# Kernel optimization log

Hardware: AMD Instinct MI355X
Metric: run time of the kernel (lower is better)

Reference implementation:

```python
import jax, jax.numpy as jnp
import numpy as np

NUM_ROUNDS = 3


def squash(x, axis=-1):
    # s_norm / (1 + s_norm) * x / sqrt(s_norm), matching the torch code exactly
    s_norm = jnp.sum(x * x, axis=axis, keepdims=True)
    return (s_norm / (1.0 + s_norm)) * x / jnp.sqrt(s_norm)


def setup_inputs() -> dict:
    key = jax.random.key(0)
    k1, k2 = jax.random.split(key)
    x = jax.random.normal(k1, (512, 1152, 8), dtype=jnp.float32)   # [B, R, Cin]
    W = jax.random.normal(k2, (10, 1152, 8, 16), dtype=jnp.float32)  # [N, R, Cin, Cout]
    return {"x": x, "W": W}


def reference(x, W):
    # priors = x[None,:,:,None,:] @ W[:,None,:,:,:]  -> [N, B, R, 1, Cout]
    priors = jnp.einsum('bri,nrio->nbro', x, W)[:, :, :, None, :]
    logits = jnp.zeros_like(priors)  # [N, B, R, 1, Cout]
    outps = None
    for i in range(NUM_ROUNDS):
        probs = jax.nn.softmax(logits, axis=2)  # softmax over routes R
        outps = squash(jnp.sum(probs * priors, axis=2, keepdims=True))  # [N, B, 1, 1, Cout]
        if i != NUM_ROUNDS - 1:
            # agreement logit update: dot over Cout
            logits = logits + jnp.sum(priors * outps, axis=-1, keepdims=True)
    return outps
```

## Files before the change

kernel.cpp:

```cpp
#include <hip/hip_runtime.h>
#include <math.h>

#define R_ROUTES 1152
#define CIN 8
#define COUT 16
#define BATCH 512
#define NCAPS 10
#define NUM_ROUNDS 3

typedef __fp16 h2 __attribute__((ext_vector_type(2)));
union U32H2 { unsigned int u; h2 h; };

__device__ __forceinline__ unsigned int pkrtz(float lo, float hi) {
    U32H2 v; v.h = __builtin_amdgcn_cvt_pkrtz(lo, hi);
    return v.u;
}
__device__ __forceinline__ h2 as_h2(unsigned int u) { U32H2 v; v.u = u; return v.h; }
__device__ __forceinline__ float f_lo(unsigned int u) { return (float)as_h2(u).x; }
__device__ __forceinline__ float f_hi(unsigned int u) { return (float)as_h2(u).y; }
__device__ __forceinline__ float dot2(unsigned int p, unsigned int s, float c) {
    return __builtin_amdgcn_fdot2(as_h2(p), as_h2(s), c, false);
}

__device__ __forceinline__ int sunit(int r, int h) {
    return (2 * r + h) ^ ((r >> 2) & 7);
}

extern "C" __global__ void __launch_bounds__(512, 4)
capsule_routing_v8(const float* __restrict__ x,
                   const float* __restrict__ W,
                   float* __restrict__ out)
{
    __shared__ unsigned int pbuf[2 * R_ROUTES * 8];
    __shared__ float red[2 * 32 * 20];
    __shared__ float sred[2 * 4];
    __shared__ float sv[2 * 16];

    const int blk = blockIdx.x;
    const int n = blk >> 8;
    const int bp = blk & 255;
    const int t = threadIdx.x;

    const float* __restrict__ x0 = x + (size_t)(2 * bp) * (R_ROUTES * CIN);
    const float* __restrict__ x1 = x0 + R_ROUTES * CIN;
    const float* __restrict__ Wn = W + (size_t)n * (R_ROUTES * CIN * COUT);

    {
        const int q = t >> 2;
        const int oq = t & 3;
        const int subw = (oq & 1) * 2;
        const int hq = oq >> 1;

        #pragma unroll 1
        for (int it = 0; it < 9; ++it) {
            const int r = it * 128 + q;
            const float4* __restrict__ wp = (const float4*)(Wn + (size_t)r * 128) + oq;
            float4 wv[8];
            #pragma unroll
            for (int i = 0; i < 8; ++i) wv[i] = wp[i * 4];
            const float4 xa0 = *(const float4*)(x0 + r * 8);
            const float4 xa1 = *(const float4*)(x0 + r * 8 + 4);
            const float4 xb0 = *(const float4*)(x1 + r * 8);
            const float4 xb1 = *(const float4*)(x1 + r * 8 + 4);

            {
                const float xs[8] = {xa0.x, xa0.y, xa0.z, xa0.w,
                                     xa1.x, xa1.y, xa1.z, xa1.w};
                float a0 = 0.f, a1 = 0.f, a2 = 0.f, a3 = 0.f;
                #pragma unroll
                for (int i = 0; i < 8; ++i) {
                    a0 = fmaf(xs[i], wv[i].x, a0);
                    a1 = fmaf(xs[i], wv[i].y, a1);
                    a2 = fmaf(xs[i], wv[i].z, a2);
                    a3 = fmaf(xs[i], wv[i].w, a3);
                }
                uint2 u; u.x = pkrtz(a0, a1); u.y = pkrtz(a2, a3);
                *(uint2*)(pbuf + sunit(r, hq) * 4 + subw) = u;
            }
            {
                const float xs[8] = {xb0.x, xb0.y, xb0.z, xb0.w,
                                     xb1.x, xb1.y, xb1.z, xb1.w};
                float a0 = 0.f, a1 = 0.f, a2 = 0.f, a3 = 0.f;
                #pragma unroll
                for (int i = 0; i < 8; ++i) {
                    a0 = fmaf(xs[i], wv[i].x, a0);
                    a1 = fmaf(xs[i], wv[i].y, a1);
                    a2 = fmaf(xs[i], wv[i].z, a2);
                    a3 = fmaf(xs[i], wv[i].w, a3);
                }
                uint2 u; u.x = pkrtz(a0, a1); u.y = pkrtz(a2, a3);
                *(uint2*)(pbuf + R_ROUTES * 8 + sunit(r, hq) * 4 + subw) = u;
            }
        }
    }
    __syncthreads();

    const int half = t >> 8;
    const int tt = t & 255;
    unsigned int* __restrict__ pb = pbuf + half * (R_ROUTES * 8);
    float* __restrict__ redh = red + half * (32 * 20);
    float* __restrict__ sredh = sred + half * 4;
    float* __restrict__ svh = sv + half * 16;

    const int nr = (tt < 128) ? 5 : 4;
    float bl[5] = {0.f, 0.f, 0.f, 0.f, 0.f};
    float factor = 0.f;

    for (int pass = 0; pass < NUM_ROUNDS; ++pass) {
        float acc[16];
        #pragma unroll
        for (int o = 0; o < 16; ++o) acc[o] = 0.f;
        float es = 0.f;

        if (pass == 0) {
            #pragma unroll
            for (int k = 0; k < 5; ++k) {
                if (k < nr) {
                    const int r = tt + (k << 8);
                    const uint4 a = *(const uint4*)(pb + sunit(r, 0) * 4);
                    const uint4 c = *(const uint4*)(pb + sunit(r, 1) * 4);
                    acc[0]  += f_lo(a.x); acc[1]  += f_hi(a.x);
                    acc[2]  += f_lo(a.y); acc[3]  += f_hi(a.y);
                    acc[4]  += f_lo(a.z); acc[5]  += f_hi(a.z);
                    acc[6]  += f_lo(a.w); acc[7]  += f_hi(a.w);
                    acc[8]  += f_lo(c.x); acc[9]  += f_hi(c.x);
                    acc[10] += f_lo(c.y); acc[11] += f_hi(c.y);
                    acc[12] += f_lo(c.z); acc[13] += f_hi(c.z);
                    acc[14] += f_lo(c.w); acc[15] += f_hi(c.w);
                }
            }
        } else {
            unsigned int svp[8];
            #pragma unroll
            for (int j = 0; j < 8; ++j)
                svp[j] = pkrtz(svh[2 * j], svh[2 * j + 1]);
            #pragma unroll
            for (int k = 0; k < 5; ++k) {
                if (k < nr) {
                    const int r = tt + (k << 8);
                    const uint4 a = *(const uint4*)(pb + sunit(r, 0) * 4);
                    const uint4 c = *(const uint4*)(pb + sunit(r, 1) * 4);
                    float d = 0.f;
                    d = dot2(a.x, svp[0], d);
                    d = dot2(a.y, svp[1], d);
                    d = dot2(a.z, svp[2], d);
                    d = dot2(a.w, svp[3], d);
                    d = dot2(c.x, svp[4], d);
                    d = dot2(c.y, svp[5], d);
                    d = dot2(c.z, svp[6], d);
                    d = dot2(c.w, svp[7], d);
                    bl[k] = fmaf(factor, d, bl[k]);
                    const float e = __expf(bl[k]);
                    es += e;
                    acc[0]  = fmaf(e, f_lo(a.x), acc[0]);
                    acc[1]  = fmaf(e, f_hi(a.x), acc[1]);
                    acc[2]  = fmaf(e, f_lo(a.y), acc[2]);
                    acc[3]  = fmaf(e, f_hi(a.y), acc[3]);
                    acc[4]  = fmaf(e, f_lo(a.z), acc[4]);
                    acc[5]  = fmaf(e, f_hi(a.z), acc[5]);
                    acc[6]  = fmaf(e, f_lo(a.w), acc[6]);
                    acc[7]  = fmaf(e, f_hi(a.w), acc[7]);
                    acc[8]  = fmaf(e, f_lo(c.x), acc[8]);
                    acc[9]  = fmaf(e, f_hi(c.x), acc[9]);
                    acc[10] = fmaf(e, f_lo(c.y), acc[10]);
                    acc[11] = fmaf(e, f_hi(c.y), acc[11]);
                    acc[12] = fmaf(e, f_lo(c.z), acc[12]);
                    acc[13] = fmaf(e, f_hi(c.z), acc[13]);
                    acc[14] = fmaf(e, f_lo(c.w), acc[14]);
                    acc[15] = fmaf(e, f_hi(c.w), acc[15]);
                }
            }
            #pragma unroll
            for (int off = 32; off > 0; off >>= 1) es += __shfl_xor(es, off, 64);
            if ((t & 63) == 0) sredh[tt >> 6] = es;
        }

        #pragma unroll
        for (int o = 0; o < 16; ++o) {
            acc[o] += __shfl_xor(acc[o], 1, 64);
            acc[o] += __shfl_xor(acc[o], 2, 64);
            acc[o] += __shfl_xor(acc[o], 4, 64);
        }
        if ((tt & 7) == 0) {
            float* dst = redh + (tt >> 3) * 20;
            *(float4*)(dst + 0)  = make_float4(acc[0],  acc[1],  acc[2],  acc[3]);
            *(float4*)(dst + 4)  = make_float4(acc[4],  acc[5],  acc[6],  acc[7]);
            *(float4*)(dst + 8)  = make_float4(acc[8],  acc[9],  acc[10], acc[11]);
            *(float4*)(dst + 12) = make_float4(acc[12], acc[13], acc[14], acc[15]);
        }
        __syncthreads();

        if (tt < 16) {
            float s = 0.f;
            #pragma unroll
            for (int w = 0; w < 32; ++w) s += redh[w * 20 + tt];
            const float Z = (pass == 0)
                ? (float)R_ROUTES
                : (sredh[0] + sredh[1] + sredh[2] + sredh[3]);
            svh[tt] = s / Z;
        }
        __syncthreads();

        float sn = 0.f;
        #pragma unroll
        for (int o = 0; o < 16; ++o) { const float s = svh[o]; sn = fmaf(s, s, sn); }
        factor = sn / ((1.0f + sn) * sqrtf(sn));
    }

    if (tt < 16)
        out[((size_t)n * BATCH + 2 * bp + half) * COUT + tt] = factor * svh[tt];
}

extern "C" void kernel_launch(void* const* d_in, const int* in_sizes, int n_in,
                              void* d_out, int out_size, void* d_ws, size_t ws_size,
                              hipStream_t stream) {
    const float* x = (const float*)d_in[0];
    const float* W = (const float*)d_in[1];
    float* out = (float*)d_out;

    dim3 grid(NCAPS * (BATCH / 2));
    dim3 block(512);
    capsule_routing_v8<<<grid, block, 0, stream>>>(x, W, out);
}
```

Measured before the change: 148.3 us.

## Pre-pack W to fp16 and compute priors with dot2, fold first routing pass

Adds a pack_w kernel that converts W to packed fp16 pairs along Cin, written into the workspace, so the main kernel loads half the W bytes per block and computes priors with fdot2 instead of fp32 FMAs. The uniform first routing pass is folded into the prior-computation loop through per-thread column sums reduced across the wave, which removes one full sweep over the shared prior buffer. Output columns are permuted to match the new per-thread output ordering. The cost is an extra kernel launch and reduced precision on x and W, which are now rounded to fp16 before the products.

```diff
diff --git a/kernel.cpp b/kernel.cpp
--- a/kernel.cpp
+++ b/kernel.cpp
@@ -26,12 +26,28 @@
     return (2 * r + h) ^ ((r >> 2) & 7);
 }
 
+extern "C" __global__ void __launch_bounds__(256)
+pack_w(const float* __restrict__ W, unsigned int* __restrict__ Wp)
+{
+    const int tau = blockIdx.x * 256 + threadIdx.x;
+    const int o = tau & 15;
+    const int nr = tau >> 4;
+    const float* __restrict__ src = W + (size_t)nr * 128 + o;
+    uint4 u;
+    u.x = pkrtz(src[0],  src[16]);
+    u.y = pkrtz(src[32], src[48]);
+    u.z = pkrtz(src[64], src[80]);
+    u.w = pkrtz(src[96], src[112]);
+    *(uint4*)(Wp + (size_t)tau * 4) = u;
+}
+
 extern "C" __global__ void __launch_bounds__(512, 4)
-capsule_routing_v8(const float* __restrict__ x,
-                   const float* __restrict__ W,
+capsule_routing_v9(const float* __restrict__ x,
+                   const unsigned int* __restrict__ Wp,
                    float* __restrict__ out)
 {
     __shared__ unsigned int pbuf[2 * R_ROUTES * 8];
+    __shared__ float wred[16 * 16];
     __shared__ float red[2 * 32 * 20];
     __shared__ float sred[2 * 4];
     __shared__ float sv[2 * 16];
@@ -43,8 +59,9 @@
 
     const float* __restrict__ x0 = x + (size_t)(2 * bp) * (R_ROUTES * CIN);
     const float* __restrict__ x1 = x0 + R_ROUTES * CIN;
-    const float* __restrict__ Wn = W + (size_t)n * (R_ROUTES * CIN * COUT);
-
+    const unsigned int* __restrict__ Wn = Wp + (size_t)n * (R_ROUTES * 64);
+
+    float cs[2][4] = {{0.f, 0.f, 0.f, 0.f}, {0.f, 0.f, 0.f, 0.f}};
     {
         const int q = t >> 2;
         const int oq = t & 3;
@@ -54,43 +71,54 @@
         #pragma unroll 1
         for (int it = 0; it < 9; ++it) {
             const int r = it * 128 + q;
-            const float4* __restrict__ wp = (const float4*)(Wn + (size_t)r * 128) + oq;
-            float4 wv[8];
-            #pragma unroll
-            for (int i = 0; i < 8; ++i) wv[i] = wp[i * 4];
+            const unsigned int* __restrict__ wb = Wn + (size_t)r * 64;
+            const uint4 w0 = *(const uint4*)(wb + (oq + 0) * 4);
+            const uint4 w1 = *(const uint4*)(wb + (oq + 4) * 4);
+            const uint4 w2 = *(const uint4*)(wb + (oq + 8) * 4);
+            const uint4 w3 = *(const uint4*)(wb + (oq + 12) * 4);
             const float4 xa0 = *(const float4*)(x0 + r * 8);
             const float4 xa1 = *(const float4*)(x0 + r * 8 + 4);
             const float4 xb0 = *(const float4*)(x1 + r * 8);
             const float4 xb1 = *(const float4*)(x1 + r * 8 + 4);
 
             {
-                const float xs[8] = {xa0.x, xa0.y, xa0.z, xa0.w,
-                                     xa1.x, xa1.y, xa1.z, xa1.w};
-                float a0 = 0.f, a1 = 0.f, a2 = 0.f, a3 = 0.f;
-                #pragma unroll
-                for (int i = 0; i < 8; ++i) {
-                    a0 = fmaf(xs[i], wv[i].x, a0);
-                    a1 = fmaf(xs[i], wv[i].y, a1);
-                    a2 = fmaf(xs[i], wv[i].z, a2);
-                    a3 = fmaf(xs[i], wv[i].w, a3);
-                }
-                uint2 u; u.x = pkrtz(a0, a1); u.y = pkrtz(a2, a3);
+                const unsigned int xp0 = pkrtz(xa0.x, xa0.y), xp1 = pkrtz(xa0.z, xa0.w);
+                const unsigned int xp2 = pkrtz(xa1.x, xa1.y), xp3 = pkrtz(xa1.z, xa1.w);
+                const float p0 = dot2(w0.w, xp3, dot2(w0.z, xp2, dot2(w0.y, xp1, dot2(w0.x, xp0, 0.f))));
+                const float p1 = dot2(w1.w, xp3, dot2(w1.z, xp2, dot2(w1.y, xp1, dot2(w1.x, xp0, 0.f))));
+                const float p2 = dot2(w2.w, xp3, dot2(w2.z, xp2, dot2(w2.y, xp1, dot2(w2.x, xp0, 0.f))));
+                const float p3 = dot2(w3.w, xp3, dot2(w3.z, xp2, dot2(w3.y, xp1, dot2(w3.x, xp0, 0.f))));
+                cs[0][0] += p0; cs[0][1] += p1; cs[0][2] += p2; cs[0][3] += p3;
+                uint2 u; u.x = pkrtz(p0, p1); u.y = pkrtz(p2, p3);
                 *(uint2*)(pbuf + sunit(r, hq) * 4 + subw) = u;
             }
             {
-                const float xs[8] = {xb0.x, xb0.y, xb0.z, xb0.w,
-                                     xb1.x, xb1.y, xb1.z, xb1.w};
-                float a0 = 0.f, a1 = 0.f, a2 = 0.f, a3 = 0.f;
-                #pragma unroll
-                for (int i = 0; i < 8; ++i) {
-                    a0 = fmaf(xs[i], wv[i].x, a0);
-                    a1 = fmaf(xs[i], wv[i].y, a1);
-                    a2 = fmaf(xs[i], wv[i].z, a2);
-                    a3 = fmaf(xs[i], wv[i].w, a3);
-                }
-                uint2 u; u.x = pkrtz(a0, a1); u.y = pkrtz(a2, a3);
+                const unsigned int xp0 = pkrtz(xb0.x, xb0.y), xp1 = pkrtz(xb0.z, xb0.w);
+                const unsigned int xp2 = pkrtz(xb1.x, xb1.y), xp3 = pkrtz(xb1.z, xb1.w);
+                const float p0 = dot2(w0.w, xp3, dot2(w0.z, xp2, dot2(w0.y, xp1, dot2(w0.x, xp0, 0.f))));
+                const float p1 = dot2(w1.w, xp3, dot2(w1.z, xp2, dot2(w1.y, xp1, dot2(w1.x, xp0, 0.f))));
+                const float p2 = dot2(w2.w, xp3, dot2(w2.z, xp2, dot2(w2.y, xp1, dot2(w2.x, xp0, 0.f))));
+                const float p3 = dot2(w3.w, xp3, dot2(w3.z, xp2, dot2(w3.y, xp1, dot2(w3.x, xp0, 0.f))));
+                cs[1][0] += p0; cs[1][1] += p1; cs[1][2] += p2; cs[1][3] += p3;
+                uint2 u; u.x = pkrtz(p0, p1); u.y = pkrtz(p2, p3);
                 *(uint2*)(pbuf + R_ROUTES * 8 + sunit(r, hq) * 4 + subw) = u;
             }
+        }
+
+        #pragma unroll
+        for (int mask = 4; mask <= 32; mask <<= 1) {
+            #pragma unroll
+            for (int b = 0; b < 2; ++b)
+                #pragma unroll
+                for (int j = 0; j < 4; ++j)
+                    cs[b][j] += __shfl_xor(cs[b][j], mask, 64);
+        }
+        if ((t & 63) < 4) {
+            const int w = t >> 6;
+            *(float4*)(wred + (w * 2 + 0) * 16 + 4 * oq) =
+                make_float4(cs[0][0], cs[0][1], cs[0][2], cs[0][3]);
+            *(float4*)(wred + (w * 2 + 1) * 16 + 4 * oq) =
+                make_float4(cs[1][0], cs[1][1], cs[1][2], cs[1][3]);
         }
     }
     __syncthreads();
@@ -102,78 +130,72 @@
     float* __restrict__ sredh = sred + half * 4;
     float* __restrict__ svh = sv + half * 16;
 
+    if (tt < 16) {
+        float s = 0.f;
+        #pragma unroll
+        for (int w = 0; w < 8; ++w) s += wred[(w * 2 + half) * 16 + tt];
+        svh[tt] = s * (1.0f / (float)R_ROUTES);
+    }
+    __syncthreads();
+
+    float sn = 0.f;
+    #pragma unroll
+    for (int o = 0; o < 16; ++o) { const float s = svh[o]; sn = fmaf(s, s, sn); }
+    float factor = sn / ((1.0f + sn) * sqrtf(sn));
+
     const int nr = (tt < 128) ? 5 : 4;
     float bl[5] = {0.f, 0.f, 0.f, 0.f, 0.f};
-    float factor = 0.f;
-
-    for (int pass = 0; pass < NUM_ROUNDS; ++pass) {
+
+    #pragma unroll 1
+    for (int pass = 1; pass < NUM_ROUNDS; ++pass) {
+        unsigned int svp[8];
+        #pragma unroll
+        for (int s = 0; s < 8; ++s)
+            svp[s] = pkrtz(svh[2 * s], svh[2 * s + 1]);
         float acc[16];
         #pragma unroll
         for (int o = 0; o < 16; ++o) acc[o] = 0.f;
         float es = 0.f;
 
-        if (pass == 0) {
-            #pragma unroll
-            for (int k = 0; k < 5; ++k) {
-                if (k < nr) {
-                    const int r = tt + (k << 8);
-                    const uint4 a = *(const uint4*)(pb + sunit(r, 0) * 4);
-                    const uint4 c = *(const uint4*)(pb + sunit(r, 1) * 4);
-                    acc[0]  += f_lo(a.x); acc[1]  += f_hi(a.x);
-                    acc[2]  += f_lo(a.y); acc[3]  += f_hi(a.y);
-                    acc[4]  += f_lo(a.z); acc[5]  += f_hi(a.z);
-                    acc[6]  += f_lo(a.w); acc[7]  += f_hi(a.w);
-                    acc[8]  += f_lo(c.x); acc[9]  += f_hi(c.x);
-                    acc[10] += f_lo(c.y); acc[11] += f_hi(c.y);
-                    acc[12] += f_lo(c.z); acc[13] += f_hi(c.z);
-                    acc[14] += f_lo(c.w); acc[15] += f_hi(c.w);
-                }
+        #pragma unroll
+        for (int k = 0; k < 5; ++k) {
+            if (k < nr) {
+                const int r = tt + (k << 8);
+                const uint4 a = *(const uint4*)(pb + sunit(r, 0) * 4);
+                const uint4 c = *(const uint4*)(pb + sunit(r, 1) * 4);
+                float d = 0.f;
+                d = dot2(a.x, svp[0], d);
+                d = dot2(a.y, svp[1], d);
+                d = dot2(a.z, svp[2], d);
+                d = dot2(a.w, svp[3], d);
+                d = dot2(c.x, svp[4], d);
+                d = dot2(c.y, svp[5], d);
+                d = dot2(c.z, svp[6], d);
+                d = dot2(c.w, svp[7], d);
+                bl[k] = fmaf(factor, d, bl[k]);
+                const float e = __expf(bl[k]);
+                es += e;
+                acc[0]  = fmaf(e, f_lo(a.x), acc[0]);
+                acc[1]  = fmaf(e, f_hi(a.x), acc[1]);
+                acc[2]  = fmaf(e, f_lo(a.y), acc[2]);
+                acc[3]  = fmaf(e, f_hi(a.y), acc[3]);
+                acc[4]  = fmaf(e, f_lo(a.z), acc[4]);
+                acc[5]  = fmaf(e, f_hi(a.z), acc[5]);
+                acc[6]  = fmaf(e, f_lo(a.w), acc[6]);
+                acc[7]  = fmaf(e, f_hi(a.w), acc[7]);
+                acc[8]  = fmaf(e, f_lo(c.x), acc[8]);
+                acc[9]  = fmaf(e, f_hi(c.x), acc[9]);
+                acc[10] = fmaf(e, f_lo(c.y), acc[10]);
+                acc[11] = fmaf(e, f_hi(c.y), acc[11]);
+                acc[12] = fmaf(e, f_lo(c.z), acc[12]);
+                acc[13] = fmaf(e, f_hi(c.z), acc[13]);
+                acc[14] = fmaf(e, f_lo(c.w), acc[14]);
+                acc[15] = fmaf(e, f_hi(c.w), acc[15]);
             }
-        } else {
-            unsigned int svp[8];
-            #pragma unroll
-            for (int j = 0; j < 8; ++j)
-                svp[j] = pkrtz(svh[2 * j], svh[2 * j + 1]);
-            #pragma unroll
-            for (int k = 0; k < 5; ++k) {
-                if (k < nr) {
-                    const int r = tt + (k << 8);
-                    const uint4 a = *(const uint4*)(pb + sunit(r, 0) * 4);
-                    const uint4 c = *(const uint4*)(pb + sunit(r, 1) * 4);
-                    float d = 0.f;
-                    d = dot2(a.x, svp[0], d);
-                    d = dot2(a.y, svp[1], d);
-                    d = dot2(a.z, svp[2], d);
-                    d = dot2(a.w, svp[3], d);
-                    d = dot2(c.x, svp[4], d);
-                    d = dot2(c.y, svp[5], d);
-                    d = dot2(c.z, svp[6], d);
-                    d = dot2(c.w, svp[7], d);
-                    bl[k] = fmaf(factor, d, bl[k]);
-                    const float e = __expf(bl[k]);
-                    es += e;
-                    acc[0]  = fmaf(e, f_lo(a.x), acc[0]);
-                    acc[1]  = fmaf(e, f_hi(a.x), acc[1]);
-                    acc[2]  = fmaf(e, f_lo(a.y), acc[2]);
-                    acc[3]  = fmaf(e, f_hi(a.y), acc[3]);
-                    acc[4]  = fmaf(e, f_lo(a.z), acc[4]);
-                    acc[5]  = fmaf(e, f_hi(a.z), acc[5]);
-                    acc[6]  = fmaf(e, f_lo(a.w), acc[6]);
-                    acc[7]  = fmaf(e, f_hi(a.w), acc[7]);
-                    acc[8]  = fmaf(e, f_lo(c.x), acc[8]);
-                    acc[9]  = fmaf(e, f_hi(c.x), acc[9]);
-                    acc[10] = fmaf(e, f_lo(c.y), acc[10]);
-                    acc[11] = fmaf(e, f_hi(c.y), acc[11]);
-                    acc[12] = fmaf(e, f_lo(c.z), acc[12]);
-                    acc[13] = fmaf(e, f_hi(c.z), acc[13]);
-                    acc[14] = fmaf(e, f_lo(c.w), acc[14]);
-                    acc[15] = fmaf(e, f_hi(c.w), acc[15]);
-                }
-            }
-            #pragma unroll
-            for (int off = 32; off > 0; off >>= 1) es += __shfl_xor(es, off, 64);
-            if ((t & 63) == 0) sredh[tt >> 6] = es;
-        }
+        }
+        #pragma unroll
+        for (int off = 32; off > 0; off >>= 1) es += __shfl_xor(es, off, 64);
+        if ((t & 63) == 0) sredh[tt >> 6] = es;
 
         #pragma unroll
         for (int o = 0; o < 16; ++o) {
@@ -194,21 +216,21 @@
             float s = 0.f;
             #pragma unroll
             for (int w = 0; w < 32; ++w) s += redh[w * 20 + tt];
-            const float Z = (pass == 0)
-                ? (float)R_ROUTES
-                : (sredh[0] + sredh[1] + sredh[2] + sredh[3]);
+            const float Z = sredh[0] + sredh[1] + sredh[2] + sredh[3];
             svh[tt] = s / Z;
         }
         __syncthreads();
 
-        float sn = 0.f;
+        sn = 0.f;
         #pragma unroll
         for (int o = 0; o < 16; ++o) { const float s = svh[o]; sn = fmaf(s, s, sn); }
         factor = sn / ((1.0f + sn) * sqrtf(sn));
     }
 
-    if (tt < 16)
-        out[((size_t)n * BATCH + 2 * bp + half) * COUT + tt] = factor * svh[tt];
+    if (tt < 16) {
+        const int o = (tt >> 2) + ((tt & 3) << 2);
+        out[((size_t)n * BATCH + 2 * bp + half) * COUT + o] = factor * svh[tt];
+    }
 }
 
 extern "C" void kernel_launch(void* const* d_in, const int* in_sizes, int n_in,
@@ -217,8 +239,8 @@
     const float* x = (const float*)d_in[0];
     const float* W = (const float*)d_in[1];
     float* out = (float*)d_out;
-
-    dim3 grid(NCAPS * (BATCH / 2));
-    dim3 block(512);
-    capsule_routing_v8<<<grid, block, 0, stream>>>(x, W, out);
-}
+    unsigned int* Wp = (unsigned int*)d_ws;
+
+    pack_w<<<dim3(NCAPS * R_ROUTES * COUT / 256), dim3(256), 0, stream>>>(W, Wp);
+    capsule_routing_v9<<<dim3(NCAPS * (BATCH / 2)), dim3(512), 0, stream>>>(x, Wp, out);
+}
```

Result: faster. 136.4 us (-8.0%).
